# Optimization experiments

Measured on AMD Instinct MI355X. Metric: run time of the kernel, lower is better.

## Reference

```python
import jax, jax.numpy as jnp
import numpy as np

TOKEN_SIZE = 16
STRIDE = 8
EMBED_DIM = 512


def setup_inputs() -> dict:
    key = jax.random.key(0)
    k1, k2 = jax.random.split(key)
    B, S, D = 32, 4096, EMBED_DIM
    x = jax.random.normal(k1, (B, S, D), dtype=jnp.float32)
    fan_in = TOKEN_SIZE * D
    W = jax.random.normal(k2, (fan_in, D), dtype=jnp.float32) / np.sqrt(fan_in)
    b = jnp.zeros((D,), dtype=jnp.float32)
    gamma = jnp.ones((D,), dtype=jnp.float32)
    beta = jnp.zeros((D,), dtype=jnp.float32)
    return {"x": x, "W": W, "b": b, "gamma": gamma, "beta": beta}


def reference(x, W, b, gamma, beta):
    B, S, D = x.shape
    n_win = (S - TOKEN_SIZE) // STRIDE + 1
    # gather all sliding windows at once: [n_win, token_size] index matrix
    idx = jnp.arange(n_win)[:, None] * STRIDE + jnp.arange(TOKEN_SIZE)[None, :]
    win = x[:, idx, :]                       # [B, n_win, token_size, D]
    win = win.reshape(B, n_win, TOKEN_SIZE * D)  # flatten each window
    h = jnp.einsum('bnf,fd->bnd', win, W) + b    # batched GEMM
    h = jax.nn.gelu(h, approximate=False)        # torch GELU default = exact erf
    # LayerNorm over last dim (eps matches torch default 1e-5)
    mu = jnp.mean(h, axis=-1, keepdims=True)
    var = jnp.var(h, axis=-1, keepdims=True)
    h = (h - mu) * jax.lax.rsqrt(var + 1e-5)
    return h * gamma + beta                      # [B, n_win, D]
```

## Files before the change

kernel.cpp:

```cpp
#include <hip/hip_runtime.h>
#include <hip/hip_bf16.h>
#include <cstdint>

#define S_LEN 4096
#define D_DIM 512
#define NWIN  511
#define KDIM  8192
#define TROWS 520
#define ASLOTS (TROWS * 8)

typedef __attribute__((ext_vector_type(8))) short short8;
typedef __attribute__((ext_vector_type(4))) float f32x4;

__device__ __forceinline__ unsigned short f2b(float f) {
    union { float f; unsigned int u; } v; v.f = f;
    unsigned int r = v.u + 0x7FFFu + ((v.u >> 16) & 1u);
    return (unsigned short)(r >> 16);
}

__global__ void wpack_kernel(const float* __restrict__ W, short8* __restrict__ pk) {
    __shared__ float tile[64][68];
    const int b2 = blockIdx.x;
    const int s = b2 >> 3, w = b2 & 7;
    const int t = s >> 3, c0 = s & 7;
    const int q = c0 * 16 + t;
    const int tid = threadIdx.x;
    {
        int r = tid >> 2, c4 = (tid & 3) << 4;
        const float* src = W + (size_t)(t * 512 + c0 * 64 + r) * D_DIM + (w << 6) + c4;
#pragma unroll
        for (int j = 0; j < 4; ++j) {
            float4 v = *(const float4*)(src + 4 * j);
            tile[r][c4 + 4 * j + 0] = v.x;
            tile[r][c4 + 4 * j + 1] = v.y;
            tile[r][c4 + 4 * j + 2] = v.z;
            tile[r][c4 + 4 * j + 3] = v.w;
        }
    }
    __syncthreads();
    const int lane = tid & 63, f2 = tid >> 6;
#pragma unroll
    for (int ff = 0; ff < 2; ++ff) {
        int f = f2 * 2 + ff;
        int n = f >> 1, k32 = f & 1;
        short8 u;
#pragma unroll
        for (int e = 0; e < 8; ++e)
            u[e] = (short)f2b(tile[k32 * 32 + (lane >> 4) * 8 + e][n * 16 + (lane & 15)]);
        pk[((size_t)q * 8 + w) * 8 * 64 + (size_t)f * 64 + lane] = u;
    }
}

__device__ __forceinline__ void load_b(const short8* __restrict__ pk, int q, int wslot,
                                       int lane, short8 (&bf)[4][2]) {
    const short8* base = pk + ((size_t)(q * 8 + wslot) * 8) * 64 + lane;
#pragma unroll
    for (int n = 0; n < 4; ++n)
#pragma unroll
        for (int k32 = 0; k32 < 2; ++k32)
            bf[n][k32] = base[(n * 2 + k32) * 64];
}

__global__ __launch_bounds__(512, 2)
void fused_kernel(const float* __restrict__ x,
                  const short8* __restrict__ pk,
                  const float* __restrict__ bias,
                  const float* __restrict__ gamma,
                  const float* __restrict__ beta,
                  float* __restrict__ out)
{
    __shared__ __align__(16) unsigned short lsA[2][TROWS * 64];
    __shared__ float redS[8][64];
    __shared__ float redQ[8][64];

    const int blk = blockIdx.x;
    const int b  = blk >> 3;
    const int n0 = (blk & 7) << 6;
    const int tid = threadIdx.x;
    const int lane = tid & 63;
    const int wid  = tid >> 6;
    const int r15 = lane & 15, hi = lane >> 4;
    const float* xb = x + (size_t)b * S_LEN * D_DIM;

    f32x4 acc[4][4] = {};
    short8 bc[4][2], bn[4][2];
    float4 ta[9][2];

#define CISSUE(J, C0N)                                                         \
    {                                                                          \
        if ((J) < 8 || tid < 64) {                                             \
            const int slot = tid + ((J) << 9);                                 \
            const int r = slot >> 3, k8 = slot & 7;                            \
            int grow = 8 * n0 + r;                                             \
            if (grow > S_LEN - 1) grow = S_LEN - 1;                            \
            const float* src = xb + (size_t)grow * D_DIM + ((C0N) << 6) + (k8 << 3); \
            ta[J][0] = *(const float4*)src;                                    \
            ta[J][1] = *(const float4*)(src + 4);                              \
        }                                                                      \
    }

#define CWRITE(J, DST)                                                         \
    {                                                                          \
        if ((J) < 8 || tid < 64) {                                             \
            const int slot = tid + ((J) << 9);                                 \
            const int r = slot >> 3, k8 = slot & 7;                            \
            short8 u;                                                          \
            u[0] = (short)f2b(ta[J][0].x); u[1] = (short)f2b(ta[J][0].y);      \
            u[2] = (short)f2b(ta[J][0].z); u[3] = (short)f2b(ta[J][0].w);      \
            u[4] = (short)f2b(ta[J][1].x); u[5] = (short)f2b(ta[J][1].y);      \
            u[6] = (short)f2b(ta[J][1].z); u[7] = (short)f2b(ta[J][1].w);      \
            *(short8*)&(DST)[(r << 6) + ((k8 ^ ((r >> 3) & 7)) << 3)] = u;     \
        }                                                                      \
    }

#define TSTEP(T, LA, BCUR, BNXT)                                               \
    {                                                                          \
        const int qn = (c0 * 16 + (T) + 1) & 127;                              \
        load_b(pk, qn, wid, lane, BNXT);                                       \
        short8 afr[4][2];                                                      \
        _Pragma("unroll")                                                      \
        for (int m = 0; m < 4; ++m) {                                          \
            const int row = (((m << 4) + r15) << 3) + (T);                     \
            const int sb  = (r15 + ((T) >> 3)) & 7;                            \
            _Pragma("unroll")                                                  \
            for (int k32 = 0; k32 < 2; ++k32)                                  \
                afr[m][k32] = *(const short8*)&(LA)[(row << 6) +               \
                                   ((((k32 << 2) + hi) ^ sb) << 3)];           \
        }                                                                      \
        _Pragma("unroll")                                                      \
        for (int k32 = 0; k32 < 2; ++k32)                                      \
            _Pragma("unroll")                                                  \
            for (int m = 0; m < 4; ++m)                                        \
                _Pragma("unroll")                                              \
                for (int n = 0; n < 4; ++n)                                    \
                    acc[m][n] = __builtin_amdgcn_mfma_f32_16x16x32_bf16(       \
                        afr[m][k32], BCUR[n][k32], acc[m][n], 0, 0, 0);        \
    }

    load_b(pk, 0, wid, lane, bc);
    CISSUE(0, 0) CISSUE(1, 0) CISSUE(2, 0) CISSUE(3, 0) CISSUE(4, 0)
    CISSUE(5, 0) CISSUE(6, 0) CISSUE(7, 0) CISSUE(8, 0)
    CWRITE(0, lsA[0]) CWRITE(1, lsA[0]) CWRITE(2, lsA[0]) CWRITE(3, lsA[0])
    CWRITE(4, lsA[0]) CWRITE(5, lsA[0]) CWRITE(6, lsA[0]) CWRITE(7, lsA[0])
    CWRITE(8, lsA[0])
    asm volatile("s_waitcnt lgkmcnt(0)" ::: "memory");
    __builtin_amdgcn_s_barrier();
    __builtin_amdgcn_sched_barrier(0);

    for (int c0 = 0; c0 < 8; ++c0) {
        const unsigned short* La = lsA[c0 & 1];
        unsigned short* Ln = lsA[(c0 + 1) & 1];
        const int c0n = c0 + 1;
        const int pf = (c0 < 7);

        TSTEP(0, La, bc, bn)
        if (pf) { CISSUE(0, c0n) CISSUE(1, c0n) }
        TSTEP(1, La, bn, bc)
        TSTEP(2, La, bc, bn)
        if (pf) { CISSUE(2, c0n) CISSUE(3, c0n) }
        TSTEP(3, La, bn, bc)
        TSTEP(4, La, bc, bn)
        if (pf) { CISSUE(4, c0n) CISSUE(5, c0n) }
        TSTEP(5, La, bn, bc)
        TSTEP(6, La, bc, bn)
        if (pf) { CISSUE(6, c0n) CISSUE(7, c0n) }
        TSTEP(7, La, bn, bc)
        TSTEP(8, La, bc, bn)
        if (pf) { CISSUE(8, c0n) CWRITE(0, Ln) CWRITE(1, Ln) }
        TSTEP(9, La, bn, bc)
        TSTEP(10, La, bc, bn)
        if (pf) { CWRITE(2, Ln) CWRITE(3, Ln) }
        TSTEP(11, La, bn, bc)
        TSTEP(12, La, bc, bn)
        if (pf) { CWRITE(4, Ln) CWRITE(5, Ln) }
        TSTEP(13, La, bn, bc)
        TSTEP(14, La, bc, bn)
        if (pf) { CWRITE(6, Ln) CWRITE(7, Ln) CWRITE(8, Ln) }
        TSTEP(15, La, bn, bc)

        asm volatile("s_waitcnt lgkmcnt(0)" ::: "memory");
        __builtin_amdgcn_s_barrier();
        __builtin_amdgcn_sched_barrier(0);
    }
#undef TSTEP
#undef CISSUE
#undef CWRITE

    float bias4[4], gam4[4], bet4[4];
#pragma unroll
    for (int n = 0; n < 4; ++n) {
        int d = (wid << 6) + 16 * n + r15;
        bias4[n] = bias[d]; gam4[n] = gamma[d]; bet4[n] = beta[d];
    }
    float sum_[4][4], sq_[4][4];
#pragma unroll
    for (int m = 0; m < 4; ++m)
#pragma unroll
        for (int r = 0; r < 4; ++r) { sum_[m][r] = 0.f; sq_[m][r] = 0.f; }
#pragma unroll
    for (int m = 0; m < 4; ++m)
#pragma unroll
        for (int n = 0; n < 4; ++n)
#pragma unroll
            for (int r = 0; r < 4; ++r) {
                float h = acc[m][n][r] + bias4[n];
                float g = 0.5f * h * (1.0f + erff(h * 0.70710678118654752f));
                acc[m][n][r] = g;
                sum_[m][r] += g;
                sq_[m][r]  += g * g;
            }
#pragma unroll
    for (int m = 0; m < 4; ++m)
#pragma unroll
        for (int r = 0; r < 4; ++r) {
            float sv = sum_[m][r], qv = sq_[m][r];
#pragma unroll
            for (int msk = 1; msk < 16; msk <<= 1) {
                sv += __shfl_xor(sv, msk, 64);
                qv += __shfl_xor(qv, msk, 64);
            }
            sum_[m][r] = sv; sq_[m][r] = qv;
        }
    if (r15 == 0) {
#pragma unroll
        for (int m = 0; m < 4; ++m)
#pragma unroll
            for (int r = 0; r < 4; ++r) {
                int row16 = 16 * m + hi * 4 + r;
                redS[wid][row16] = sum_[m][r];
                redQ[wid][row16] = sq_[m][r];
            }
    }
    __syncthreads();
#pragma unroll
    for (int m = 0; m < 4; ++m) {
#pragma unroll
        for (int r = 0; r < 4; ++r) {
            int row16 = 16 * m + hi * 4 + r;
            float sv = 0.f, qv = 0.f;
#pragma unroll
            for (int w = 0; w < 8; ++w) { sv += redS[w][row16]; qv += redQ[w][row16]; }
            float mu  = sv * (1.0f / 512.0f);
            float var = qv * (1.0f / 512.0f) - mu * mu;
            float inv = rsqrtf(var + 1e-5f);
            int win = n0 + row16;
            if (win < NWIN) {
                size_t obase = ((size_t)b * NWIN + win) * D_DIM;
#pragma unroll
                for (int n = 0; n < 4; ++n) {
                    int d = (wid << 6) + 16 * n + r15;
                    out[obase + d] = (acc[m][n][r] - mu) * inv * gam4[n] + bet4[n];
                }
            }
        }
    }
}

__global__ void naive_kernel(const float* __restrict__ x, const float* __restrict__ W,
                             const float* __restrict__ bias, const float* __restrict__ gamma,
                             const float* __restrict__ beta, float* __restrict__ out) {
    __shared__ float hrow[D_DIM];
    __shared__ float red[2];
    const int b = blockIdx.x / NWIN, win = blockIdx.x % NWIN;
    const int d = threadIdx.x;
    float a = 0.f;
    for (int t = 0; t < 16; ++t) {
        const float* xr = x + ((size_t)b * S_LEN + 8 * win + t) * D_DIM;
        const float* wr = W + (size_t)t * D_DIM * D_DIM;
        for (int k = 0; k < D_DIM; ++k) a += xr[k] * wr[(size_t)k * D_DIM + d];
    }
    a += bias[d];
    a = 0.5f * a * (1.0f + erff(a * 0.70710678118654752f));
    hrow[d] = a;
    __syncthreads();
    if (d == 0) {
        float s = 0.f, q = 0.f;
        for (int k = 0; k < D_DIM; ++k) { s += hrow[k]; q += hrow[k] * hrow[k]; }
        float mu = s / D_DIM;
        red[0] = mu; red[1] = rsqrtf(q / D_DIM - mu * mu + 1e-5f);
    }
    __syncthreads();
    out[((size_t)b * NWIN + win) * D_DIM + d] = (a - red[0]) * red[1] * gamma[d] + beta[d];
}

extern "C" void kernel_launch(void* const* d_in, const int* in_sizes, int n_in,
                              void* d_out, int out_size, void* d_ws, size_t ws_size,
                              hipStream_t stream) {
    const float* x     = (const float*)d_in[0];
    const float* W     = (const float*)d_in[1];
    const float* bias  = (const float*)d_in[2];
    const float* gamma = (const float*)d_in[3];
    const float* beta  = (const float*)d_in[4];
    float* out = (float*)d_out;

    const size_t pk_bytes = (size_t)KDIM * D_DIM * sizeof(unsigned short);
    if (ws_size >= pk_bytes) {
        short8* pk = (short8*)d_ws;
        wpack_kernel<<<1024, 256, 0, stream>>>(W, pk);
        fused_kernel<<<256, 512, 0, stream>>>(x, pk, bias, gamma, beta, out);
    } else {
        naive_kernel<<<32 * NWIN, D_DIM, 0, stream>>>(x, W, bias, gamma, beta, out);
    }
}
```

Measured before the change: 176.5 us.

## Deepen B-fragment prefetch to two steps and restructure A staging swizzle

Keeps four B register buffers so the weight fragments are prefetched two t-steps ahead instead of one. The x-tile staging is interleaved (issue, then convert and write) with only two in-flight float4 pairs, which reduces register pressure. The LDS layout switches to a 16-slot, 8-byte-granular XOR swizzle that also depends on row parity, with A fragments read as two 64-bit halves. Launch bounds drop to one block per CU minimum, which gives the compiler more registers but may lower occupancy.

```diff
diff --git a/kernel.cpp b/kernel.cpp
--- a/kernel.cpp
+++ b/kernel.cpp
@@ -10,6 +10,7 @@
 #define ASLOTS (TROWS * 8)
 
 typedef __attribute__((ext_vector_type(8))) short short8;
+typedef __attribute__((ext_vector_type(4))) short short4v;
 typedef __attribute__((ext_vector_type(4))) float f32x4;
 
 __device__ __forceinline__ unsigned short f2b(float f) {
@@ -61,7 +62,7 @@
             bf[n][k32] = base[(n * 2 + k32) * 64];
 }
 
-__global__ __launch_bounds__(512, 2)
+__global__ __launch_bounds__(512, 1)
 void fused_kernel(const float* __restrict__ x,
                   const short8* __restrict__ pk,
                   const float* __restrict__ bias,
@@ -83,8 +84,8 @@
     const float* xb = x + (size_t)b * S_LEN * D_DIM;
 
     f32x4 acc[4][4] = {};
-    short8 bc[4][2], bn[4][2];
-    float4 ta[9][2];
+    short8 b0[4][2], b1[4][2], b2[4][2], b3[4][2];
+    float4 ta[2][2];
 
 #define CISSUE(J, C0N)                                                         \
     {                                                                          \
@@ -94,8 +95,8 @@
             int grow = 8 * n0 + r;                                             \
             if (grow > S_LEN - 1) grow = S_LEN - 1;                            \
             const float* src = xb + (size_t)grow * D_DIM + ((C0N) << 6) + (k8 << 3); \
-            ta[J][0] = *(const float4*)src;                                    \
-            ta[J][1] = *(const float4*)(src + 4);                              \
+            ta[(J) & 1][0] = *(const float4*)src;                              \
+            ta[(J) & 1][1] = *(const float4*)(src + 4);                        \
         }                                                                      \
     }
 
@@ -104,28 +105,37 @@
         if ((J) < 8 || tid < 64) {                                             \
             const int slot = tid + ((J) << 9);                                 \
             const int r = slot >> 3, k8 = slot & 7;                            \
-            short8 u;                                                          \
-            u[0] = (short)f2b(ta[J][0].x); u[1] = (short)f2b(ta[J][0].y);      \
-            u[2] = (short)f2b(ta[J][0].z); u[3] = (short)f2b(ta[J][0].w);      \
-            u[4] = (short)f2b(ta[J][1].x); u[5] = (short)f2b(ta[J][1].y);      \
-            u[6] = (short)f2b(ta[J][1].z); u[7] = (short)f2b(ta[J][1].w);      \
-            *(short8*)&(DST)[(r << 6) + ((k8 ^ ((r >> 3) & 7)) << 3)] = u;     \
+            const int sw = ((r >> 3) & 15) ^ (r & 1);                          \
+            short4v lo, hi4;                                                   \
+            lo[0] = (short)f2b(ta[(J) & 1][0].x);                              \
+            lo[1] = (short)f2b(ta[(J) & 1][0].y);                              \
+            lo[2] = (short)f2b(ta[(J) & 1][0].z);                              \
+            lo[3] = (short)f2b(ta[(J) & 1][0].w);                              \
+            hi4[0] = (short)f2b(ta[(J) & 1][1].x);                             \
+            hi4[1] = (short)f2b(ta[(J) & 1][1].y);                             \
+            hi4[2] = (short)f2b(ta[(J) & 1][1].z);                             \
+            hi4[3] = (short)f2b(ta[(J) & 1][1].w);                             \
+            *(short4v*)&(DST)[(r << 6) + ((((k8 << 1)) ^ sw) << 2)]     = lo;  \
+            *(short4v*)&(DST)[(r << 6) + ((((k8 << 1) | 1) ^ sw) << 2)] = hi4; \
         }                                                                      \
     }
 
-#define TSTEP(T, LA, BCUR, BNXT)                                               \
+#define TSTEP(T, LA, BU, BL)                                                   \
     {                                                                          \
-        const int qn = (c0 * 16 + (T) + 1) & 127;                              \
-        load_b(pk, qn, wid, lane, BNXT);                                       \
+        const int qn = (c0 * 16 + (T) + 2) & 127;                              \
+        load_b(pk, qn, wid, lane, BL);                                         \
+        const int swr = ((r15 + ((T) >> 3)) & 15) ^ ((T) & 1);                 \
         short8 afr[4][2];                                                      \
         _Pragma("unroll")                                                      \
         for (int m = 0; m < 4; ++m) {                                          \
             const int row = (((m << 4) + r15) << 3) + (T);                     \
-            const int sb  = (r15 + ((T) >> 3)) & 7;                            \
             _Pragma("unroll")                                                  \
-            for (int k32 = 0; k32 < 2; ++k32)                                  \
-                afr[m][k32] = *(const short8*)&(LA)[(row << 6) +               \
-                                   ((((k32 << 2) + hi) ^ sb) << 3)];           \
+            for (int k32 = 0; k32 < 2; ++k32) {                                \
+                const int sl = (k32 << 3) + (hi << 1);                         \
+                short4v alo = *(const short4v*)&(LA)[(row << 6) + ((sl ^ swr) << 2)];        \
+                short4v ahi = *(const short4v*)&(LA)[(row << 6) + (((sl | 1) ^ swr) << 2)];  \
+                afr[m][k32] = __builtin_shufflevector(alo, ahi, 0, 1, 2, 3, 4, 5, 6, 7);     \
+            }                                                                  \
         }                                                                      \
         _Pragma("unroll")                                                      \
         for (int k32 = 0; k32 < 2; ++k32)                                      \
@@ -134,15 +144,16 @@
                 _Pragma("unroll")                                              \
                 for (int n = 0; n < 4; ++n)                                    \
                     acc[m][n] = __builtin_amdgcn_mfma_f32_16x16x32_bf16(       \
-                        afr[m][k32], BCUR[n][k32], acc[m][n], 0, 0, 0);        \
-    }
-
-    load_b(pk, 0, wid, lane, bc);
-    CISSUE(0, 0) CISSUE(1, 0) CISSUE(2, 0) CISSUE(3, 0) CISSUE(4, 0)
-    CISSUE(5, 0) CISSUE(6, 0) CISSUE(7, 0) CISSUE(8, 0)
-    CWRITE(0, lsA[0]) CWRITE(1, lsA[0]) CWRITE(2, lsA[0]) CWRITE(3, lsA[0])
-    CWRITE(4, lsA[0]) CWRITE(5, lsA[0]) CWRITE(6, lsA[0]) CWRITE(7, lsA[0])
-    CWRITE(8, lsA[0])
+                        afr[m][k32], BU[n][k32], acc[m][n], 0, 0, 0);          \
+    }
+
+    load_b(pk, 0, wid, lane, b0);
+    load_b(pk, 1, wid, lane, b1);
+    CISSUE(0, 0) CWRITE(0, lsA[0]) CISSUE(1, 0) CWRITE(1, lsA[0])
+    CISSUE(2, 0) CWRITE(2, lsA[0]) CISSUE(3, 0) CWRITE(3, lsA[0])
+    CISSUE(4, 0) CWRITE(4, lsA[0]) CISSUE(5, 0) CWRITE(5, lsA[0])
+    CISSUE(6, 0) CWRITE(6, lsA[0]) CISSUE(7, 0) CWRITE(7, lsA[0])
+    CISSUE(8, 0) CWRITE(8, lsA[0])
     asm volatile("s_waitcnt lgkmcnt(0)" ::: "memory");
     __builtin_amdgcn_s_barrier();
     __builtin_amdgcn_sched_barrier(0);
@@ -153,30 +164,32 @@
         const int c0n = c0 + 1;
         const int pf = (c0 < 7);
 
-        TSTEP(0, La, bc, bn)
+        TSTEP(0, La, b0, b2)
         if (pf) { CISSUE(0, c0n) CISSUE(1, c0n) }
-        TSTEP(1, La, bn, bc)
-        TSTEP(2, La, bc, bn)
-        if (pf) { CISSUE(2, c0n) CISSUE(3, c0n) }
-        TSTEP(3, La, bn, bc)
-        TSTEP(4, La, bc, bn)
-        if (pf) { CISSUE(4, c0n) CISSUE(5, c0n) }
-        TSTEP(5, La, bn, bc)
-        TSTEP(6, La, bc, bn)
-        if (pf) { CISSUE(6, c0n) CISSUE(7, c0n) }
-        TSTEP(7, La, bn, bc)
-        TSTEP(8, La, bc, bn)
-        if (pf) { CISSUE(8, c0n) CWRITE(0, Ln) CWRITE(1, Ln) }
-        TSTEP(9, La, bn, bc)
-        TSTEP(10, La, bc, bn)
-        if (pf) { CWRITE(2, Ln) CWRITE(3, Ln) }
-        TSTEP(11, La, bn, bc)
-        TSTEP(12, La, bc, bn)
-        if (pf) { CWRITE(4, Ln) CWRITE(5, Ln) }
-        TSTEP(13, La, bn, bc)
-        TSTEP(14, La, bc, bn)
-        if (pf) { CWRITE(6, Ln) CWRITE(7, Ln) CWRITE(8, Ln) }
-        TSTEP(15, La, bn, bc)
+        TSTEP(1, La, b1, b3)
+        if (pf) { CWRITE(0, Ln) CISSUE(2, c0n) }
+        TSTEP(2, La, b2, b0)
+        if (pf) { CWRITE(1, Ln) CISSUE(3, c0n) }
+        TSTEP(3, La, b3, b1)
+        if (pf) { CWRITE(2, Ln) CISSUE(4, c0n) }
+        TSTEP(4, La, b0, b2)
+        if (pf) { CWRITE(3, Ln) CISSUE(5, c0n) }
+        TSTEP(5, La, b1, b3)
+        if (pf) { CWRITE(4, Ln) CISSUE(6, c0n) }
+        TSTEP(6, La, b2, b0)
+        if (pf) { CWRITE(5, Ln) CISSUE(7, c0n) }
+        TSTEP(7, La, b3, b1)
+        if (pf) { CWRITE(6, Ln) CISSUE(8, c0n) }
+        TSTEP(8, La, b0, b2)
+        if (pf) { CWRITE(7, Ln) }
+        TSTEP(9, La, b1, b3)
+        if (pf) { CWRITE(8, Ln) }
+        TSTEP(10, La, b2, b0)
+        TSTEP(11, La, b3, b1)
+        TSTEP(12, La, b0, b2)
+        TSTEP(13, La, b1, b3)
+        TSTEP(14, La, b2, b0)
+        TSTEP(15, La, b3, b1)
 
         asm volatile("s_waitcnt lgkmcnt(0)" ::: "memory");
         __builtin_amdgcn_s_barrier();
```

After: 205.4 us. 16.4% more time.

## Split GEMM along K into two halves with separate GELU+LayerNorm reduction kernel

Applied to the files above, without the earlier changes.

Replaces the single fused GEMM+epilogue kernel with a split-K GEMM that launches twice as many blocks, each covering half of the reduction dimension, at higher occupancy (launch bounds 4 blocks). Partial results go to a workspace, and a new row-wise kernel sums the two partials and applies bias, exact GELU and LayerNorm. The aim is to fill the GPU better, since the original grid of 256 blocks underused the compute units. The cost is roughly 67 MB of extra fp32 partial traffic written and read back, plus an extra launch. The new path runs only when the workspace is large enough, otherwise it falls back to the old fused path.

```diff
diff --git a/kernel.cpp b/kernel.cpp
--- a/kernel.cpp
+++ b/kernel.cpp
@@ -6,11 +6,15 @@
 #define D_DIM 512
 #define NWIN  511
 #define KDIM  8192
-#define TROWS 520
-#define ASLOTS (TROWS * 8)
+#define TR5   520
+#define ROWB  72
+#define TR6   520
 
 typedef __attribute__((ext_vector_type(8))) short short8;
+typedef __attribute__((ext_vector_type(4))) short short4v;
 typedef __attribute__((ext_vector_type(4))) float f32x4;
+
+#define PH_ELEMS ((size_t)32 * NWIN * D_DIM)
 
 __device__ __forceinline__ unsigned short f2b(float f) {
     union { float f; unsigned int u; } v; v.f = f;
@@ -18,7 +22,238 @@
     return (unsigned short)(r >> 16);
 }
 
-__global__ void wpack_kernel(const float* __restrict__ W, short8* __restrict__ pk) {
+__global__ void wpack2_kernel(const float* __restrict__ W, short8* __restrict__ pk) {
+    __shared__ float tile[64][68];
+    const int b2 = blockIdx.x;
+    const int s = b2 >> 3, w = b2 & 7;
+    const int t = s >> 3, c0 = s & 7;
+    const int tid = threadIdx.x;
+    {
+        int r = tid >> 2, c4 = (tid & 3) << 4;
+        const float* src = W + (size_t)(t * 512 + c0 * 64 + r) * D_DIM + (w << 6) + c4;
+#pragma unroll
+        for (int j = 0; j < 4; ++j) {
+            float4 v = *(const float4*)(src + 4 * j);
+            tile[r][c4 + 4 * j + 0] = v.x;
+            tile[r][c4 + 4 * j + 1] = v.y;
+            tile[r][c4 + 4 * j + 2] = v.z;
+            tile[r][c4 + 4 * j + 3] = v.w;
+        }
+    }
+    __syncthreads();
+    const int lane = tid & 63, f2 = tid >> 6;
+    const int r15 = lane & 15, hi = lane >> 4;
+#pragma unroll
+    for (int ff = 0; ff < 2; ++ff) {
+        int f = f2 * 2 + ff;
+        int n = f >> 1, k32 = f & 1;
+        int q2 = (c0 * 2 + k32) * 16 + t;
+        short8 u;
+#pragma unroll
+        for (int e = 0; e < 8; ++e)
+            u[e] = (short)f2b(tile[k32 * 32 + hi * 8 + e][n * 16 + r15]);
+        pk[(size_t)q2 * 2048 + w * 256 + n * 64 + lane] = u;
+    }
+}
+
+__global__ __launch_bounds__(512, 4)
+void gemm5_kernel(const float* __restrict__ x,
+                  const short8* __restrict__ pk,
+                  float* __restrict__ ph)
+{
+    __shared__ __align__(16) unsigned char lsA[2][TR5 * ROWB];
+
+    const int bid = blockIdx.x;
+    const int kh  = (bid & 7) >> 2;
+    const int g   = ((bid >> 3) << 2) | (bid & 3);
+    const int b   = g >> 3;
+    const int n0  = (g & 7) << 6;
+    const int tid = threadIdx.x;
+    const int lane = tid & 63, wc = tid >> 6;
+    const int r15 = lane & 15, hi = lane >> 4;
+    const int boff = (wc << 8) + lane;
+    const int khb = kh << 7;
+    const float* xb = x + (size_t)b * S_LEN * D_DIM;
+
+    f32x4 acc[4][4] = {};
+    short8 Bc[4], Bn[4];
+    float4 ta[2][2];
+
+#define CISSUE(J, S)                                                           \
+    {                                                                          \
+        if ((J) < 4 || tid < 32) {                                             \
+            const int c_ = tid + ((J) << 9);                                   \
+            const int r_ = c_ >> 2, k4_ = c_ & 3;                              \
+            int gr_ = (n0 << 3) + r_;                                          \
+            if (gr_ > S_LEN - 1) gr_ = S_LEN - 1;                              \
+            const float* s_ = xb + (size_t)gr_ * D_DIM + (kh * 256 + (S) * 32) + (k4_ << 3); \
+            ta[(J) & 1][0] = *(const float4*)s_;                               \
+            ta[(J) & 1][1] = *(const float4*)(s_ + 4);                         \
+        }                                                                      \
+    }
+
+#define CWRITE(J, DST)                                                         \
+    {                                                                          \
+        if ((J) < 4 || tid < 32) {                                             \
+            const int c_ = tid + ((J) << 9);                                   \
+            const int r_ = c_ >> 2, k4_ = c_ & 3;                              \
+            const int sw_ = ((r_ >> 3) & 7) ^ ((r_ >> 6) & 1);                 \
+            short4v lo_, hh_;                                                  \
+            lo_[0] = (short)f2b(ta[(J) & 1][0].x);                             \
+            lo_[1] = (short)f2b(ta[(J) & 1][0].y);                             \
+            lo_[2] = (short)f2b(ta[(J) & 1][0].z);                             \
+            lo_[3] = (short)f2b(ta[(J) & 1][0].w);                             \
+            hh_[0] = (short)f2b(ta[(J) & 1][1].x);                             \
+            hh_[1] = (short)f2b(ta[(J) & 1][1].y);                             \
+            hh_[2] = (short)f2b(ta[(J) & 1][1].z);                             \
+            hh_[3] = (short)f2b(ta[(J) & 1][1].w);                             \
+            *(short4v*)&(DST)[r_ * ROWB + ((((k4_ << 1)    ) ^ sw_) << 3)] = lo_; \
+            *(short4v*)&(DST)[r_ * ROWB + ((((k4_ << 1) | 1) ^ sw_) << 3)] = hh_; \
+        }                                                                      \
+    }
+
+#define TSTEP(T, LA, BU, BL)                                                   \
+    {                                                                          \
+        const int q2n = khb + ((s16 + (T) + 1) & 127);                         \
+        _Pragma("unroll")                                                      \
+        for (int n = 0; n < 4; ++n)                                            \
+            BL[n] = pk[(size_t)q2n * 2048 + boff + n * 64];                    \
+        __builtin_amdgcn_s_setprio(1);                                         \
+        _Pragma("unroll")                                                      \
+        for (int m = 0; m < 4; ++m) {                                          \
+            const int r_ = (((m << 4) + r15) << 3) + (T);                      \
+            const int sw_ = ((r_ >> 3) & 7) ^ ((r_ >> 6) & 1);                 \
+            const unsigned char* rb_ = (LA) + r_ * ROWB;                       \
+            short4v alo = *(const short4v*)&rb_[(((hi << 1)    ) ^ sw_) << 3]; \
+            short4v ahi = *(const short4v*)&rb_[(((hi << 1) | 1) ^ sw_) << 3]; \
+            short8 afr = __builtin_shufflevector(alo, ahi, 0, 1, 2, 3, 4, 5, 6, 7); \
+            _Pragma("unroll")                                                  \
+            for (int n = 0; n < 4; ++n)                                        \
+                acc[m][n] = __builtin_amdgcn_mfma_f32_16x16x32_bf16(           \
+                    afr, BU[n], acc[m][n], 0, 0, 0);                           \
+        }                                                                      \
+        __builtin_amdgcn_s_setprio(0);                                         \
+    }
+
+#pragma unroll
+    for (int n = 0; n < 4; ++n)
+        Bc[n] = pk[(size_t)khb * 2048 + boff + n * 64];
+    CISSUE(0, 0) CISSUE(1, 0) CWRITE(0, lsA[0]) CISSUE(2, 0) CWRITE(1, lsA[0])
+    CISSUE(3, 0) CWRITE(2, lsA[0]) CISSUE(4, 0) CWRITE(3, lsA[0]) CWRITE(4, lsA[0])
+    asm volatile("s_waitcnt lgkmcnt(0)" ::: "memory");
+    __builtin_amdgcn_s_barrier();
+    __builtin_amdgcn_sched_barrier(0);
+
+    for (int s = 0; s < 8; ++s) {
+        const unsigned char* La = lsA[s & 1];
+        unsigned char* Ln = lsA[(s + 1) & 1];
+        const int s16 = s << 4;
+        const int sn = s + 1;
+        const int pf = (s < 7);
+
+        TSTEP(0, La, Bc, Bn)
+        if (pf) CISSUE(0, sn)
+        TSTEP(1, La, Bn, Bc)
+        if (pf) CISSUE(1, sn)
+        TSTEP(2, La, Bc, Bn)
+        if (pf) { CWRITE(0, Ln) CISSUE(2, sn) }
+        TSTEP(3, La, Bn, Bc)
+        if (pf) { CWRITE(1, Ln) CISSUE(3, sn) }
+        TSTEP(4, La, Bc, Bn)
+        if (pf) { CWRITE(2, Ln) CISSUE(4, sn) }
+        TSTEP(5, La, Bn, Bc)
+        if (pf) CWRITE(3, Ln)
+        TSTEP(6, La, Bc, Bn)
+        if (pf) CWRITE(4, Ln)
+        TSTEP(7, La, Bn, Bc)
+        TSTEP(8, La, Bc, Bn)
+        TSTEP(9, La, Bn, Bc)
+        TSTEP(10, La, Bc, Bn)
+        TSTEP(11, La, Bn, Bc)
+        TSTEP(12, La, Bc, Bn)
+        TSTEP(13, La, Bn, Bc)
+        TSTEP(14, La, Bc, Bn)
+        TSTEP(15, La, Bn, Bc)
+
+        asm volatile("s_waitcnt lgkmcnt(0)" ::: "memory");
+        __builtin_amdgcn_s_barrier();
+        __builtin_amdgcn_sched_barrier(0);
+    }
+#undef TSTEP
+#undef CISSUE
+#undef CWRITE
+
+    float* hb = ph + (size_t)kh * PH_ELEMS + (size_t)b * NWIN * D_DIM;
+#pragma unroll
+    for (int m = 0; m < 4; ++m) {
+#pragma unroll
+        for (int r = 0; r < 4; ++r) {
+            int win = n0 + (m << 4) + (hi << 2) + r;
+            if (win < NWIN) {
+                float* dst = hb + (size_t)win * D_DIM + (wc << 6) + r15;
+#pragma unroll
+                for (int n = 0; n < 4; ++n)
+                    dst[n << 4] = acc[m][n][r];
+            }
+        }
+    }
+}
+
+__global__ __launch_bounds__(256, 8)
+void ln2_kernel(const float* __restrict__ ph, const float* __restrict__ bias,
+                const float* __restrict__ gamma, const float* __restrict__ beta,
+                float* __restrict__ out, int nrows)
+{
+    const int lane = threadIdx.x & 63;
+    const int wv = blockIdx.x * 4 + (threadIdx.x >> 6);
+    const int nw = gridDim.x * 4;
+    float bi[8], gm[8], bt[8];
+#pragma unroll
+    for (int j = 0; j < 8; ++j) {
+        bi[j] = bias[lane * 8 + j];
+        gm[j] = gamma[lane * 8 + j];
+        bt[j] = beta[lane * 8 + j];
+    }
+    for (int row = wv; row < nrows; row += nw) {
+        const float* s0 = ph + (size_t)row * D_DIM + lane * 8;
+        const float* s1 = s0 + PH_ELEMS;
+        float4 a0 = *(const float4*)s0;
+        float4 a1 = *(const float4*)(s0 + 4);
+        float4 b0 = *(const float4*)s1;
+        float4 b1 = *(const float4*)(s1 + 4);
+        float v[8] = { a0.x + b0.x, a0.y + b0.y, a0.z + b0.z, a0.w + b0.w,
+                       a1.x + b1.x, a1.y + b1.y, a1.z + b1.z, a1.w + b1.w };
+        float s = 0.f, q = 0.f;
+#pragma unroll
+        for (int j = 0; j < 8; ++j) {
+            float h = v[j] + bi[j];
+            float gl = 0.5f * h * (1.0f + erff(h * 0.70710678118654752f));
+            v[j] = gl;
+            s += gl; q += gl * gl;
+        }
+#pragma unroll
+        for (int msk = 1; msk < 64; msk <<= 1) {
+            s += __shfl_xor(s, msk, 64);
+            q += __shfl_xor(q, msk, 64);
+        }
+        float mu  = s * (1.0f / 512.0f);
+        float inv = rsqrtf(q * (1.0f / 512.0f) - mu * mu + 1e-5f);
+        float4 r0, r1;
+        r0.x = (v[0] - mu) * inv * gm[0] + bt[0];
+        r0.y = (v[1] - mu) * inv * gm[1] + bt[1];
+        r0.z = (v[2] - mu) * inv * gm[2] + bt[2];
+        r0.w = (v[3] - mu) * inv * gm[3] + bt[3];
+        r1.x = (v[4] - mu) * inv * gm[4] + bt[4];
+        r1.y = (v[5] - mu) * inv * gm[5] + bt[5];
+        r1.z = (v[6] - mu) * inv * gm[6] + bt[6];
+        r1.w = (v[7] - mu) * inv * gm[7] + bt[7];
+        float* dst = out + (size_t)row * D_DIM + lane * 8;
+        *(float4*)dst = r0;
+        *(float4*)(dst + 4) = r1;
+    }
+}
+
+__global__ void wpack_c0_kernel(const float* __restrict__ W, short8* __restrict__ pk) {
     __shared__ float tile[64][68];
     const int b2 = blockIdx.x;
     const int s = b2 >> 3, w = b2 & 7;
@@ -51,8 +286,8 @@
     }
 }
 
-__device__ __forceinline__ void load_b(const short8* __restrict__ pk, int q, int wslot,
-                                       int lane, short8 (&bf)[4][2]) {
+__device__ __forceinline__ void load_b8(const short8* __restrict__ pk, int q, int wslot,
+                                        int lane, short8 (&bf)[4][2]) {
     const short8* base = pk + ((size_t)(q * 8 + wslot) * 8) * 64 + lane;
 #pragma unroll
     for (int n = 0; n < 4; ++n)
@@ -62,14 +297,14 @@
 }
 
 __global__ __launch_bounds__(512, 2)
-void fused_kernel(const float* __restrict__ x,
-                  const short8* __restrict__ pk,
-                  const float* __restrict__ bias,
-                  const float* __restrict__ gamma,
-                  const float* __restrict__ beta,
-                  float* __restrict__ out)
+void fusedR6_kernel(const float* __restrict__ x,
+                    const short8* __restrict__ pk,
+                    const float* __restrict__ bias,
+                    const float* __restrict__ gamma,
+                    const float* __restrict__ beta,
+                    float* __restrict__ out)
 {
-    __shared__ __align__(16) unsigned short lsA[2][TROWS * 64];
+    __shared__ __align__(16) unsigned short lsA6[2][TR6 * 64];
     __shared__ float redS[8][64];
     __shared__ float redQ[8][64];
 
@@ -86,7 +321,7 @@
     short8 bc[4][2], bn[4][2];
     float4 ta[9][2];
 
-#define CISSUE(J, C0N)                                                         \
+#define FCISSUE(J, C0N)                                                        \
     {                                                                          \
         if ((J) < 8 || tid < 64) {                                             \
             const int slot = tid + ((J) << 9);                                 \
@@ -99,7 +334,7 @@
         }                                                                      \
     }
 
-#define CWRITE(J, DST)                                                         \
+#define FCWRITE(J, DST)                                                        \
     {                                                                          \
         if ((J) < 8 || tid < 64) {                                             \
             const int slot = tid + ((J) << 9);                                 \
@@ -113,10 +348,10 @@
         }                                                                      \
     }
 
-#define TSTEP(T, LA, BCUR, BNXT)                                               \
+#define FTSTEP(T, LA, BCUR, BNXT)                                              \
     {                                                                          \
         const int qn = (c0 * 16 + (T) + 1) & 127;                              \
-        load_b(pk, qn, wid, lane, BNXT);                                       \
+        load_b8(pk, qn, wid, lane, BNXT);                                      \
         short8 afr[4][2];                                                      \
         _Pragma("unroll")                                                      \
         for (int m = 0; m < 4; ++m) {                                          \
@@ -137,54 +372,54 @@
                         afr[m][k32], BCUR[n][k32], acc[m][n], 0, 0, 0);        \
     }
 
-    load_b(pk, 0, wid, lane, bc);
-    CISSUE(0, 0) CISSUE(1, 0) CISSUE(2, 0) CISSUE(3, 0) CISSUE(4, 0)
-    CISSUE(5, 0) CISSUE(6, 0) CISSUE(7, 0) CISSUE(8, 0)
-    CWRITE(0, lsA[0]) CWRITE(1, lsA[0]) CWRITE(2, lsA[0]) CWRITE(3, lsA[0])
-    CWRITE(4, lsA[0]) CWRITE(5, lsA[0]) CWRITE(6, lsA[0]) CWRITE(7, lsA[0])
-    CWRITE(8, lsA[0])
+    load_b8(pk, 0, wid, lane, bc);
+    FCISSUE(0, 0) FCISSUE(1, 0) FCISSUE(2, 0) FCISSUE(3, 0) FCISSUE(4, 0)
+    FCISSUE(5, 0) FCISSUE(6, 0) FCISSUE(7, 0) FCISSUE(8, 0)
+    FCWRITE(0, lsA6[0]) FCWRITE(1, lsA6[0]) FCWRITE(2, lsA6[0]) FCWRITE(3, lsA6[0])
+    FCWRITE(4, lsA6[0]) FCWRITE(5, lsA6[0]) FCWRITE(6, lsA6[0]) FCWRITE(7, lsA6[0])
+    FCWRITE(8, lsA6[0])
     asm volatile("s_waitcnt lgkmcnt(0)" ::: "memory");
     __builtin_amdgcn_s_barrier();
     __builtin_amdgcn_sched_barrier(0);
 
     for (int c0 = 0; c0 < 8; ++c0) {
-        const unsigned short* La = lsA[c0 & 1];
-        unsigned short* Ln = lsA[(c0 + 1) & 1];
+        const unsigned short* La = lsA6[c0 & 1];
+        unsigned short* Ln = lsA6[(c0 + 1) & 1];
         const int c0n = c0 + 1;
         const int pf = (c0 < 7);
 
-        TSTEP(0, La, bc, bn)
-        if (pf) { CISSUE(0, c0n) CISSUE(1, c0n) }
-        TSTEP(1, La, bn, bc)
-        TSTEP(2, La, bc, bn)
-        if (pf) { CISSUE(2, c0n) CISSUE(3, c0n) }
-        TSTEP(3, La, bn, bc)
-        TSTEP(4, La, bc, bn)
-        if (pf) { CISSUE(4, c0n) CISSUE(5, c0n) }
-        TSTEP(5, La, bn, bc)
-        TSTEP(6, La, bc, bn)
-        if (pf) { CISSUE(6, c0n) CISSUE(7, c0n) }
-        TSTEP(7, La, bn, bc)
-        TSTEP(8, La, bc, bn)
-        if (pf) { CISSUE(8, c0n) CWRITE(0, Ln) CWRITE(1, Ln) }
-        TSTEP(9, La, bn, bc)
-        TSTEP(10, La, bc, bn)
-        if (pf) { CWRITE(2, Ln) CWRITE(3, Ln) }
-        TSTEP(11, La, bn, bc)
-        TSTEP(12, La, bc, bn)
-        if (pf) { CWRITE(4, Ln) CWRITE(5, Ln) }
-        TSTEP(13, La, bn, bc)
-        TSTEP(14, La, bc, bn)
-        if (pf) { CWRITE(6, Ln) CWRITE(7, Ln) CWRITE(8, Ln) }
-        TSTEP(15, La, bn, bc)
+        FTSTEP(0, La, bc, bn)
+        if (pf) { FCISSUE(0, c0n) FCISSUE(1, c0n) }
+        FTSTEP(1, La, bn, bc)
+        FTSTEP(2, La, bc, bn)
+        if (pf) { FCISSUE(2, c0n) FCISSUE(3, c0n) }
+        FTSTEP(3, La, bn, bc)
+        FTSTEP(4, La, bc, bn)
+        if (pf) { FCISSUE(4, c0n) FCISSUE(5, c0n) }
+        FTSTEP(5, La, bn, bc)
+        FTSTEP(6, La, bc, bn)
+        if (pf) { FCISSUE(6, c0n) FCISSUE(7, c0n) }
+        FTSTEP(7, La, bn, bc)
+        FTSTEP(8, La, bc, bn)
+        if (pf) { FCISSUE(8, c0n) FCWRITE(0, Ln) FCWRITE(1, Ln) }
+        FTSTEP(9, La, bn, bc)
+        FTSTEP(10, La, bc, bn)
+        if (pf) { FCWRITE(2, Ln) FCWRITE(3, Ln) }
+        FTSTEP(11, La, bn, bc)
+        FTSTEP(12, La, bc, bn)
+        if (pf) { FCWRITE(4, Ln) FCWRITE(5, Ln) }
+        FTSTEP(13, La, bn, bc)
+        FTSTEP(14, La, bc, bn)
+        if (pf) { FCWRITE(6, Ln) FCWRITE(7, Ln) FCWRITE(8, Ln) }
+        FTSTEP(15, La, bn, bc)
 
         asm volatile("s_waitcnt lgkmcnt(0)" ::: "memory");
         __builtin_amdgcn_s_barrier();
         __builtin_amdgcn_sched_barrier(0);
     }
-#undef TSTEP
-#undef CISSUE
-#undef CWRITE
+#undef FTSTEP
+#undef FCISSUE
+#undef FCWRITE
 
     float bias4[4], gam4[4], bet4[4];
 #pragma unroll
@@ -294,10 +529,18 @@
     float* out = (float*)d_out;
 
     const size_t pk_bytes = (size_t)KDIM * D_DIM * sizeof(unsigned short);
-    if (ws_size >= pk_bytes) {
+    const size_t ph_bytes = 2 * PH_ELEMS * sizeof(float);
+
+    if (ws_size >= pk_bytes + ph_bytes) {
         short8* pk = (short8*)d_ws;
-        wpack_kernel<<<1024, 256, 0, stream>>>(W, pk);
-        fused_kernel<<<256, 512, 0, stream>>>(x, pk, bias, gamma, beta, out);
+        float* ph = (float*)((char*)d_ws + pk_bytes);
+        wpack2_kernel<<<1024, 256, 0, stream>>>(W, pk);
+        gemm5_kernel<<<512, 512, 0, stream>>>(x, pk, ph);
+        ln2_kernel<<<1024, 256, 0, stream>>>(ph, bias, gamma, beta, out, 32 * NWIN);
+    } else if (ws_size >= pk_bytes) {
+        short8* pk = (short8*)d_ws;
+        wpack_c0_kernel<<<1024, 256, 0, stream>>>(W, pk);
+        fusedR6_kernel<<<256, 512, 0, stream>>>(x, pk, bias, gamma, beta, out);
     } else {
         naive_kernel<<<32 * NWIN, D_DIM, 0, stream>>>(x, W, bias, gamma, beta, out);
     }
```

Result: slower. 353.6 us (+100.3%).
